# Kernel tuning notes

Measured on AMD Instinct MI355X. Metric: run time of the kernel, lower is better.

Reference implementation:

```python
import jax, jax.numpy as jnp
import numpy as np

D_MODEL = 1024
NUM_HEADS = 16
D_K = D_MODEL // NUM_HEADS
B, S = 2, 2048
NEG = -1e9


def setup_inputs() -> dict:
    key = jax.random.key(0)
    ks = jax.random.split(key, 12)
    sc = 1.0 / np.sqrt(D_MODEL)
    inp = {
        'Q': jax.random.normal(ks[0], (B, S, D_MODEL), jnp.float32),
        'K': jax.random.normal(ks[1], (B, S, D_MODEL), jnp.float32),
        'V': jax.random.normal(ks[2], (B, S, D_MODEL), jnp.float32),
        # causal additive mask: 1.0 above diagonal -> scores += mask * -1e9
        'mask': jnp.triu(jnp.ones((S, S), jnp.float32), k=1),
        'Wq': jax.random.normal(ks[3], (D_MODEL, D_MODEL), jnp.float32) * sc,
        'bq': jnp.zeros((D_MODEL,), jnp.float32),
        'Wk': jax.random.normal(ks[4], (D_MODEL, D_MODEL), jnp.float32) * sc,
        'bk': jnp.zeros((D_MODEL,), jnp.float32),
        'Wv': jax.random.normal(ks[5], (D_MODEL, D_MODEL), jnp.float32) * sc,
        'bv': jnp.zeros((D_MODEL,), jnp.float32),
        'Wo': jax.random.normal(ks[6], (D_MODEL, D_MODEL), jnp.float32) * sc,
        'bo': jnp.zeros((D_MODEL,), jnp.float32),
    }
    return inp


def _split_heads(x):
    # [B,S,D] -> [B,H,S,d_k]
    b, s, _ = x.shape
    return x.reshape(b, s, NUM_HEADS, D_K).transpose(0, 2, 1, 3)


def reference(Q, K, V, mask, Wq, bq, Wk, bk, Wv, bv, Wo, bo):
    # torch Linear: y = x @ W.T + b
    q = _split_heads(Q @ Wq.T + bq)  # [B,H,S,d_k]
    k = _split_heads(K @ Wk.T + bk)
    v = _split_heads(V @ Wv.T + bv)
    scores = jnp.einsum('bhqd,bhkd->bhqk', q, k) / np.sqrt(D_K)
    scores = scores + mask * NEG  # mask broadcasts over [B,H]
    probs = jax.nn.softmax(scores, axis=-1)
    attn = jnp.einsum('bhqk,bhkd->bhqd', probs, v)  # [B,H,S,d_k]
    attn = attn.transpose(0, 2, 1, 3).reshape(Q.shape[0], Q.shape[1], D_MODEL)
    return attn @ Wo.T + bo
```

## Files before the change

### kernel.cpp

```cpp
#include <hip/hip_runtime.h>
#include <cstdint>
#include <cstddef>

#define D_MODEL 1024
#define NHEADS  16
#define DK      64
#define BATCH   2
#define SEQ     2048
#define MTOT    (BATCH*SEQ)
#define NT      (SEQ/64)

typedef unsigned short u16;
typedef __attribute__((ext_vector_type(8))) __bf16 bf16x8;
typedef __attribute__((ext_vector_type(4))) float  f32x4;
typedef __attribute__((ext_vector_type(4))) uint32_t u32x4;

#define QSCALE 0.18033688f

static __device__ __forceinline__ void gload16(const void* g, void* l) {
  __builtin_amdgcn_global_load_lds((const __attribute__((address_space(1))) void*)g,
                                   (__attribute__((address_space(3))) void*)l,
                                   16, 0, 0);
}

__global__ void cast_all_kernel(
    const float* __restrict__ Q, const float* __restrict__ K, const float* __restrict__ V,
    const float* __restrict__ Wq, const float* __restrict__ Wk,
    const float* __restrict__ Wv, const float* __restrict__ Wo,
    u16* __restrict__ dstX, u16* __restrict__ dstW) {
  constexpr int NX = MTOT * D_MODEL;
  constexpr int NW = D_MODEL * D_MODEL;
  const int i = (blockIdx.x * blockDim.x + threadIdx.x) * 4;
  const float* src;
  u16* dst;
  if (i < 3 * NX) {
    dst = dstX + i;
    src = (i < NX) ? Q + i : (i < 2 * NX) ? K + (i - NX) : V + (i - 2 * NX);
  } else {
    const int j = i - 3 * NX;
    dst = dstW + j;
    const int ws = j >> 20;
    const int jo = j & (NW - 1);
    src = (ws == 0) ? Wq + jo : (ws == 1) ? Wk + jo : (ws == 2) ? Wv + jo : Wo + jo;
  }
  float4 f = *reinterpret_cast<const float4*>(src);
  union { __bf16 h[4]; ushort4 s; } o;
  o.h[0] = (__bf16)f.x; o.h[1] = (__bf16)f.y; o.h[2] = (__bf16)f.z; o.h[3] = (__bf16)f.w;
  *reinterpret_cast<ushort4*>(dst) = o.s;
}

__global__ __launch_bounds__(256, 2) void gemm_qkv(
    const u16* __restrict__ A,
    const u16* __restrict__ W0, const u16* __restrict__ W1, const u16* __restrict__ W2,
    const float* __restrict__ b0, const float* __restrict__ b1, const float* __restrict__ b2,
    u16* __restrict__ out_q, u16* __restrict__ out_k, u16* __restrict__ out_v) {
  constexpr int K = 1024;
  __shared__ __align__(16) u16 lA[128 * 64];
  __shared__ __align__(16) u16 lB[128 * 64];
  const int w = threadIdx.x >> 6, lane = threadIdx.x & 63;
  const int blockM = blockIdx.x * 128, blockN = blockIdx.y * 128;
  const int sel = blockIdx.x >> 5;
  const u16*  Bt   = sel == 0 ? W0 : (sel == 1 ? W1 : W2);
  const float* bias = sel == 0 ? b0 : (sel == 1 ? b1 : b2);
  const int wm = (w >> 1) * 64, wn = (w & 1) * 64;
  f32x4 acc[4][4] = {};
  for (int kt = 0; kt < K; kt += 64) {
#pragma unroll
    for (int it = 0; it < 4; ++it) {
      int rowb = w * 32 + it * 8;
      int row  = rowb + (lane >> 3);
      int cc   = (lane & 7) * 8;
      gload16(A  + (size_t)(blockM + row) * K + kt + cc, &lA[rowb * 64]);
      gload16(Bt + (size_t)(blockN + row) * K + kt + cc, &lB[rowb * 64]);
    }
    __syncthreads();
#pragma unroll
    for (int kc = 0; kc < 2; ++kc) {
      bf16x8 af[4], bfr[4];
#pragma unroll
      for (int i = 0; i < 4; ++i)
        af[i] = *(const bf16x8*)&lA[(wm + i * 16 + (lane & 15)) * 64 + kc * 32 + (lane >> 4) * 8];
#pragma unroll
      for (int j = 0; j < 4; ++j)
        bfr[j] = *(const bf16x8*)&lB[(wn + j * 16 + (lane & 15)) * 64 + kc * 32 + (lane >> 4) * 8];
#pragma unroll
      for (int i = 0; i < 4; ++i)
#pragma unroll
        for (int j = 0; j < 4; ++j)
          acc[i][j] = __builtin_amdgcn_mfma_f32_16x16x32_bf16(af[i], bfr[j], acc[i][j], 0, 0, 0);
    }
    __syncthreads();
  }
  if (sel == 2) {
#pragma unroll
    for (int i = 0; i < 4; ++i)
#pragma unroll
      for (int j = 0; j < 4; ++j) {
        int m0 = blockM + wm + i * 16 + (lane >> 4) * 4;
        int n  = blockN + wn + j * 16 + (lane & 15);
        int ml = m0 & (MTOT - 1);
        int b = ml >> 11, s = ml & (SEQ - 1), h = n >> 6, d = n & (DK - 1);
        union { __bf16 h4[4]; ushort4 s4; } st;
#pragma unroll
        for (int r = 0; r < 4; ++r) st.h4[r] = (__bf16)(acc[i][j][r] + bias[n]);
        *(ushort4*)&out_v[(((size_t)(b * NHEADS + h)) * DK + d) * SEQ + s] = st.s4;
      }
  } else {
    u16* outqk = sel ? out_k : out_q;
#pragma unroll
    for (int i = 0; i < 4; ++i)
#pragma unroll
      for (int j = 0; j < 4; ++j)
#pragma unroll
        for (int r = 0; r < 4; ++r) {
          int m = blockM + wm + i * 16 + (lane >> 4) * 4 + r;
          int n = blockN + wn + j * 16 + (lane & 15);
          float val = acc[i][j][r] + bias[n];
          if (sel == 0) val *= QSCALE;
          int ml = m & (MTOT - 1);
          int b = ml >> 11, s = ml & (SEQ - 1), h = n >> 6, d = n & (DK - 1);
          u16 bv; { union { __bf16 h2; u16 u; } cv; cv.h2 = (__bf16)val; bv = cv.u; }
          outqk[(((size_t)(b * NHEADS + h)) * SEQ + s) * DK + d] = bv;
        }
  }
}

__global__ __launch_bounds__(256, 2) void gemm_out(
    const u16* __restrict__ A, const u16* __restrict__ Bt,
    const float* __restrict__ bias, float* __restrict__ outp) {
  constexpr int K = 1024, N = 1024;
  __shared__ __align__(16) u16 lA[64 * 64];
  __shared__ __align__(16) u16 lB[128 * 64];
  const int w = threadIdx.x >> 6, lane = threadIdx.x & 63;
  const int blockM = blockIdx.x * 64, blockN = blockIdx.y * 128;
  const int wm = (w >> 1) * 32, wn = (w & 1) * 64;
  f32x4 acc[2][4] = {};
  for (int kt = 0; kt < K; kt += 64) {
#pragma unroll
    for (int it = 0; it < 2; ++it) {
      int rowb = w * 16 + it * 8;
      int row  = rowb + (lane >> 3);
      int cc   = (lane & 7) * 8;
      gload16(A + (size_t)(blockM + row) * K + kt + cc, &lA[rowb * 64]);
    }
#pragma unroll
    for (int it = 0; it < 4; ++it) {
      int rowb = w * 32 + it * 8;
      int row  = rowb + (lane >> 3);
      int cc   = (lane & 7) * 8;
      gload16(Bt + (size_t)(blockN + row) * K + kt + cc, &lB[rowb * 64]);
    }
    __syncthreads();
#pragma unroll
    for (int kc = 0; kc < 2; ++kc) {
      bf16x8 af[2], bfr[4];
#pragma unroll
      for (int i = 0; i < 2; ++i)
        af[i] = *(const bf16x8*)&lA[(wm + i * 16 + (lane & 15)) * 64 + kc * 32 + (lane >> 4) * 8];
#pragma unroll
      for (int j = 0; j < 4; ++j)
        bfr[j] = *(const bf16x8*)&lB[(wn + j * 16 + (lane & 15)) * 64 + kc * 32 + (lane >> 4) * 8];
#pragma unroll
      for (int i = 0; i < 2; ++i)
#pragma unroll
        for (int j = 0; j < 4; ++j)
          acc[i][j] = __builtin_amdgcn_mfma_f32_16x16x32_bf16(af[i], bfr[j], acc[i][j], 0, 0, 0);
    }
    __syncthreads();
  }
#pragma unroll
  for (int i = 0; i < 2; ++i)
#pragma unroll
    for (int j = 0; j < 4; ++j)
#pragma unroll
      for (int r = 0; r < 4; ++r) {
        int m = blockM + wm + i * 16 + (lane >> 4) * 4 + r;
        int n = blockN + wn + j * 16 + (lane & 15);
        outp[(size_t)m * N + n] = acc[i][j][r] + bias[n];
      }
}

static __device__ __forceinline__ void stage_kv(
    const u16* kp, const u16* vp, int j0,
    u16* bufK, u16* bufV, int w, int lane) {
  const int rsub = lane >> 3;
  const int cl = ((lane & 7) ^ rsub) << 3;
#pragma unroll
  for (int it = 0; it < 2; ++it) {
    const int rowb = w * 16 + it * 8;
    gload16(kp + (size_t)(j0 + rowb + rsub) * DK + cl, bufK + rowb * 64);
    gload16(vp + (size_t)(rowb + rsub) * SEQ + j0 + cl, bufV + rowb * 64);
  }
}

__global__ __launch_bounds__(256, 4) void attn_kernel(
    const u16* __restrict__ qh, const u16* __restrict__ kh,
    const u16* __restrict__ vt, u16* __restrict__ attnb) {
  __shared__ __align__(16) u16 lKV[2][2][64 * 64];
  const int w = threadIdx.x >> 6, lane = threadIdx.x & 63;
  const int g = lane >> 4, q15 = lane & 15;
  const int lid = blockIdx.x;
  const int xcd = lid & 7;
  const int local = lid >> 3;
  const int cu = local & 31;
  const int p  = local >> 5;
  const int bh = xcd * 4 + p;
  const int cb = (p & 2) ? ((cu + 8) & 31) : cu;
  const int qt = (p & 1) ? (NT - 1 - cb) : cb;
  const int b = bh >> 4, h = bh & 15;
  const u16* qp = qh + (size_t)bh * SEQ * DK;
  const u16* kp = kh + (size_t)bh * SEQ * DK;
  const u16* vp = vt + (size_t)bh * DK * SEQ;

  const int qbase = qt * 64;
  const int qrow = qbase + w * 16 + q15;
  bf16x8 aq[2];
  const u16* qr = qp + (size_t)qrow * DK;
#pragma unroll
  for (int kc = 0; kc < 2; ++kc)
    aq[kc] = *(const bf16x8*)(qr + kc * 32 + g * 8);

  float m_run = -1e30f, l_run = 0.f;
  f32x4 oacc[4] = {};
  const int nt = qt + 1;
  stage_kv(kp, vp, 0, lKV[0][0], lKV[0][1], w, lane);

  for (int t = 0; t < nt; ++t) {
    __syncthreads();
    const int cur = t & 1;
    if (t + 1 < nt)
      stage_kv(kp, vp, (t + 1) * 64, lKV[cur ^ 1][0], lKV[cur ^ 1][1], w, lane);
    const u16* bK = lKV[cur][0];
    const u16* bV = lKV[cur][1];

    f32x4 sacc[4] = {};
    __builtin_amdgcn_s_setprio(1);
#pragma unroll
    for (int kc = 0; kc < 2; ++kc)
#pragma unroll
      for (int nb = 0; nb < 4; ++nb) {
        const int rr = nb * 16 + q15;
        const int cc = kc * 4 + g;
        bf16x8 kf = *(const bf16x8*)&bK[rr * 64 + ((cc ^ (rr & 7)) << 3)];
        sacc[nb] = __builtin_amdgcn_mfma_f32_16x16x32_bf16(kf, aq[kc], sacc[nb], 0, 0, 0);
      }
    __builtin_amdgcn_s_setprio(0);

    float pvv[4][4];
    float mx = -1e30f;
    if (t == qt) {
#pragma unroll
      for (int nb = 0; nb < 4; ++nb)
#pragma unroll
        for (int r = 0; r < 4; ++r) {
          float s = sacc[nb][r];
          if (t * 64 + nb * 16 + g * 4 + r > qrow) s = -1e30f;
          pvv[nb][r] = s;
          mx = fmaxf(mx, s);
        }
    } else {
#pragma unroll
      for (int nb = 0; nb < 4; ++nb)
#pragma unroll
        for (int r = 0; r < 4; ++r) {
          float s = sacc[nb][r];
          pvv[nb][r] = s;
          mx = fmaxf(mx, s);
        }
    }
    mx = fmaxf(mx, __shfl_xor(mx, 16));
    mx = fmaxf(mx, __shfl_xor(mx, 32));
    if (__any(mx > m_run + 8.0f)) {
      const float mn = fmaxf(m_run, mx);
      const float alpha = __builtin_amdgcn_exp2f(m_run - mn);
      m_run = mn;
      l_run *= alpha;
#pragma unroll
      for (int nd = 0; nd < 4; ++nd)
#pragma unroll
        for (int r = 0; r < 4; ++r) oacc[nd][r] *= alpha;
    }
    float rs = 0.f;
#pragma unroll
    for (int nb = 0; nb < 4; ++nb)
#pragma unroll
      for (int r = 0; r < 4; ++r) {
        float e = __builtin_amdgcn_exp2f(pvv[nb][r] - m_run);
        pvv[nb][r] = e;
        rs += e;
      }
    rs += __shfl_xor(rs, 16);
    rs += __shfl_xor(rs, 32);
    l_run += rs;

    uint32_t pk[4][2];
#pragma unroll
    for (int nb = 0; nb < 4; ++nb) {
      union { __bf16 h2[2]; uint32_t u; } t0, t1;
      t0.h2[0] = (__bf16)pvv[nb][0]; t0.h2[1] = (__bf16)pvv[nb][1];
      t1.h2[0] = (__bf16)pvv[nb][2]; t1.h2[1] = (__bf16)pvv[nb][3];
      pk[nb][0] = t0.u; pk[nb][1] = t1.u;
    }

#pragma unroll
    for (int jc = 0; jc < 2; ++jc) {
      union { u32x4 u; bf16x8 bvec; } pf;
      const int sgbase = (g & 1) * 2;
#pragma unroll
      for (int W = 0; W < 4; ++W) {
        const int src = (sgbase + (W >> 1)) * 16 + q15;
        const uint32_t lo = (uint32_t)__shfl((int)pk[2 * jc][W & 1], src, 64);
        const uint32_t hi = (uint32_t)__shfl((int)pk[2 * jc + 1][W & 1], src, 64);
        pf.u[W] = (lane >= 32) ? hi : lo;
      }
      __builtin_amdgcn_s_setprio(1);
#pragma unroll
      for (int nd = 0; nd < 4; ++nd) {
        const int rr = nd * 16 + q15;
        const int cc = jc * 4 + g;
        bf16x8 vf = *(const bf16x8*)&bV[rr * 64 + ((cc ^ (rr & 7)) << 3)];
        oacc[nd] = __builtin_amdgcn_mfma_f32_16x16x32_bf16(vf, pf.bvec, oacc[nd], 0, 0, 0);
      }
      __builtin_amdgcn_s_setprio(0);
    }
  }

  const float rl = 1.0f / l_run;
#pragma unroll
  for (int nd = 0; nd < 4; ++nd) {
    union { __bf16 h4[4]; ushort4 s4; } st;
    st.h4[0] = (__bf16)(oacc[nd][0] * rl);
    st.h4[1] = (__bf16)(oacc[nd][1] * rl);
    st.h4[2] = (__bf16)(oacc[nd][2] * rl);
    st.h4[3] = (__bf16)(oacc[nd][3] * rl);
    *(ushort4*)&attnb[((size_t)(b * SEQ + qrow)) * D_MODEL + h * 64 + nd * 16 + g * 4] = st.s4;
  }
}

extern "C" void kernel_launch(void* const* d_in, const int* in_sizes, int n_in,
                              void* d_out, int out_size, void* d_ws, size_t ws_size,
                              hipStream_t stream) {
  (void)in_sizes; (void)n_in; (void)out_size; (void)ws_size;
  const float* Q  = (const float*)d_in[0];
  const float* K  = (const float*)d_in[1];
  const float* V  = (const float*)d_in[2];
  const float* Wq = (const float*)d_in[4];
  const float* bq = (const float*)d_in[5];
  const float* Wk = (const float*)d_in[6];
  const float* bk = (const float*)d_in[7];
  const float* Wv = (const float*)d_in[8];
  const float* bv = (const float*)d_in[9];
  const float* Wo = (const float*)d_in[10];
  const float* bo = (const float*)d_in[11];

  char* ws = (char*)d_ws;
  size_t off = 0;
  auto carve = [&](size_t bytes) { char* p = ws + off; off += bytes; return p; };
  const size_t szX = (size_t)MTOT * D_MODEL * 2;
  const size_t szW = (size_t)D_MODEL * D_MODEL * 2;
  u16* Qb  = (u16*)carve(szX);
  u16* Kb  = (u16*)carve(szX);
  u16* Vb  = (u16*)carve(szX);
  u16* Wqb = (u16*)carve(szW);
  u16* Wkb = (u16*)carve(szW);
  u16* Wvb = (u16*)carve(szW);
  u16* Wob = (u16*)carve(szW);
  u16* qhB = (u16*)carve(szX);
  u16* khB = (u16*)carve(szX);
  u16* vtB = (u16*)carve(szX);
  u16* attnb = Qb;
  (void)Kb; (void)Vb; (void)Wkb; (void)Wvb; (void)Wob;

  const int nTot = 3 * MTOT * D_MODEL + 4 * D_MODEL * D_MODEL;
  cast_all_kernel<<<nTot / 1024, 256, 0, stream>>>(Q, K, V, Wq, Wk, Wv, Wo, Qb, Wqb);

  gemm_qkv<<<dim3(3 * MTOT / 128, D_MODEL / 128), 256, 0, stream>>>(
      Qb, Wqb, Wkb, Wvb, bq, bk, bv, qhB, khB, vtB);

  attn_kernel<<<NT * BATCH * NHEADS, 256, 0, stream>>>(qhB, khB, vtB, attnb);

  gemm_out<<<dim3(MTOT / 64, D_MODEL / 128), 256, 0, stream>>>(attnb, Wob, bo, (float*)d_out);
}
```

Baseline: 121.9 us.

## Split long causal query tiles across two blocks and merge with combine kernel

Query tiles 16..31 (the longest causal rows) are now split into two halves of the KV range, each handled by its own block, which writes unnormalized partial outputs plus running max and sum to fp32 scratch. A new combine kernel merges the two partials with log-sum-exp weights and writes bf16 output. The goal is to balance per-block work and shorten the tail of the attention grid. The cost is an extra kernel launch, extra global traffic for the fp32 partials, and reuse of the Kb and Wqb workspace as scratch.

Result: no change. 122.8 us (+0.7%).

```diff
diff --git a/kernel.cpp b/kernel.cpp
--- a/kernel.cpp
+++ b/kernel.cpp
@@ -195,18 +195,27 @@
 
 __global__ __launch_bounds__(256, 4) void attn_kernel(
     const u16* __restrict__ qh, const u16* __restrict__ kh,
-    const u16* __restrict__ vt, u16* __restrict__ attnb) {
+    const u16* __restrict__ vt, u16* __restrict__ attnb,
+    float* __restrict__ pO, float* __restrict__ pML) {
   __shared__ __align__(16) u16 lKV[2][2][64 * 64];
   const int w = threadIdx.x >> 6, lane = threadIdx.x & 63;
   const int g = lane >> 4, q15 = lane & 15;
   const int lid = blockIdx.x;
   const int xcd = lid & 7;
-  const int local = lid >> 3;
-  const int cu = local & 31;
-  const int p  = local >> 5;
+  const int idx = lid >> 3;
+  const int p   = idx & 3;
+  const int slot = idx >> 2;
   const int bh = xcd * 4 + p;
-  const int cb = (p & 2) ? ((cu + 8) & 31) : cu;
-  const int qt = (p & 1) ? (NT - 1 - cb) : cb;
+  int qt, t_begin, t_end, half, split;
+  if (slot < 32) {
+    qt = 16 + (slot >> 1); half = slot & 1; split = 1;
+    const int ntt = qt + 1, h0 = ntt >> 1;
+    t_begin = half ? h0 : 0;
+    t_end   = half ? ntt : h0;
+  } else {
+    qt = 47 - slot; half = 0; split = 0;
+    t_begin = 0; t_end = qt + 1;
+  }
   const int b = bh >> 4, h = bh & 15;
   const u16* qp = qh + (size_t)bh * SEQ * DK;
   const u16* kp = kh + (size_t)bh * SEQ * DK;
@@ -222,13 +231,12 @@
 
   float m_run = -1e30f, l_run = 0.f;
   f32x4 oacc[4] = {};
-  const int nt = qt + 1;
-  stage_kv(kp, vp, 0, lKV[0][0], lKV[0][1], w, lane);
-
-  for (int t = 0; t < nt; ++t) {
+  stage_kv(kp, vp, t_begin * 64, lKV[t_begin & 1][0], lKV[t_begin & 1][1], w, lane);
+
+  for (int t = t_begin; t < t_end; ++t) {
     __syncthreads();
     const int cur = t & 1;
-    if (t + 1 < nt)
+    if (t + 1 < t_end)
       stage_kv(kp, vp, (t + 1) * 64, lKV[cur ^ 1][0], lKV[cur ^ 1][1], w, lane);
     const u16* bK = lKV[cur][0];
     const u16* bV = lKV[cur][1];
@@ -325,15 +333,60 @@
     }
   }
 
-  const float rl = 1.0f / l_run;
-#pragma unroll
-  for (int nd = 0; nd < 4; ++nd) {
+  if (!split) {
+    const float rl = 1.0f / l_run;
+#pragma unroll
+    for (int nd = 0; nd < 4; ++nd) {
+      union { __bf16 h4[4]; ushort4 s4; } st;
+      st.h4[0] = (__bf16)(oacc[nd][0] * rl);
+      st.h4[1] = (__bf16)(oacc[nd][1] * rl);
+      st.h4[2] = (__bf16)(oacc[nd][2] * rl);
+      st.h4[3] = (__bf16)(oacc[nd][3] * rl);
+      *(ushort4*)&attnb[((size_t)(b * SEQ + qrow)) * D_MODEL + h * 64 + nd * 16 + g * 4] = st.s4;
+    }
+  } else {
+    const int pid = ((bh << 4) + (qt - 16)) * 2 + half;
+    float* po = pO + (size_t)pid * 4096 + (w * 16 + q15) * 64;
+#pragma unroll
+    for (int nd = 0; nd < 4; ++nd)
+      *(f32x4*)(po + nd * 16 + g * 4) = oacc[nd];
+    if (g == 0) {
+      float2 ml; ml.x = m_run; ml.y = l_run;
+      ((float2*)pML)[pid * 64 + w * 16 + q15] = ml;
+    }
+  }
+}
+
+__global__ __launch_bounds__(256) void attn_combine(
+    const float* __restrict__ pO, const float* __restrict__ pML,
+    u16* __restrict__ attnb) {
+  const int blk = blockIdx.x;
+  const int bh = blk >> 4, qti = blk & 15;
+  const int qt = 16 + qti;
+  const int b = bh >> 4, h = bh & 15;
+  const int pid0 = ((bh << 4) + qti) * 2;
+  const int t = threadIdx.x;
+  const int row = t >> 2, c0 = (t & 3) * 16;
+  const float2 ml0 = ((const float2*)pML)[pid0 * 64 + row];
+  const float2 ml1 = ((const float2*)pML)[(pid0 + 1) * 64 + row];
+  const float M = fmaxf(ml0.x, ml1.x);
+  const float w0 = __builtin_amdgcn_exp2f(ml0.x - M);
+  const float w1 = __builtin_amdgcn_exp2f(ml1.x - M);
+  const float inv = 1.0f / (ml0.y * w0 + ml1.y * w1);
+  const float s0 = w0 * inv, s1 = w1 * inv;
+  const float* O0 = pO + (size_t)pid0 * 4096 + row * 64 + c0;
+  const float* O1 = O0 + 4096;
+  u16* dst = attnb + ((size_t)(b * SEQ + qt * 64 + row)) * D_MODEL + h * 64 + c0;
+#pragma unroll
+  for (int c = 0; c < 4; ++c) {
+    float4 a  = *(const float4*)(O0 + c * 4);
+    float4 d2 = *(const float4*)(O1 + c * 4);
     union { __bf16 h4[4]; ushort4 s4; } st;
-    st.h4[0] = (__bf16)(oacc[nd][0] * rl);
-    st.h4[1] = (__bf16)(oacc[nd][1] * rl);
-    st.h4[2] = (__bf16)(oacc[nd][2] * rl);
-    st.h4[3] = (__bf16)(oacc[nd][3] * rl);
-    *(ushort4*)&attnb[((size_t)(b * SEQ + qrow)) * D_MODEL + h * 64 + nd * 16 + g * 4] = st.s4;
+    st.h4[0] = (__bf16)(a.x * s0 + d2.x * s1);
+    st.h4[1] = (__bf16)(a.y * s0 + d2.y * s1);
+    st.h4[2] = (__bf16)(a.z * s0 + d2.z * s1);
+    st.h4[3] = (__bf16)(a.w * s0 + d2.w * s1);
+    *(ushort4*)(dst + c * 4) = st.s4;
   }
 }
 
@@ -369,7 +422,9 @@
   u16* khB = (u16*)carve(szX);
   u16* vtB = (u16*)carve(szX);
   u16* attnb = Qb;
-  (void)Kb; (void)Vb; (void)Wkb; (void)Wvb; (void)Wob;
+  float* pO  = (float*)Kb;
+  float* pML = (float*)Wqb;
+  (void)Wkb; (void)Wvb;
 
   const int nTot = 3 * MTOT * D_MODEL + 4 * D_MODEL * D_MODEL;
   cast_all_kernel<<<nTot / 1024, 256, 0, stream>>>(Q, K, V, Wq, Wk, Wv, Wo, Qb, Wqb);
@@ -377,7 +432,9 @@
   gemm_qkv<<<dim3(3 * MTOT / 128, D_MODEL / 128), 256, 0, stream>>>(
       Qb, Wqb, Wkb, Wvb, bq, bk, bv, qhB, khB, vtB);
 
-  attn_kernel<<<NT * BATCH * NHEADS, 256, 0, stream>>>(qhB, khB, vtB, attnb);
+  attn_kernel<<<1536, 256, 0, stream>>>(qhB, khB, vtB, attnb, pO, pML);
+
+  attn_combine<<<512, 256, 0, stream>>>(pO, pML, attnb);
 
   gemm_out<<<dim3(MTOT / 64, D_MODEL / 128), 256, 0, stream>>>(attnb, Wob, bo, (float*)d_out);
 }
```
